# Optimization experiments

Measured on AMD Instinct MI355X. Metric: run time of the kernel, lower is better.

Reference implementation:

```python
import jax, jax.numpy as jnp
import numpy as np

STRIDES = (4.0, 8.0, 16.0, 32.0)
IMG = 1024.0


def setup_inputs() -> dict:
    key = jax.random.key(0)
    ks = jax.random.split(key, 10)
    N, P = 512, 128
    feat0 = jax.random.normal(ks[0], (2, 256, 256, 256), jnp.float32)
    feat1 = jax.random.normal(ks[1], (2, 256, 128, 128), jnp.float32)
    feat2 = jax.random.normal(ks[2], (2, 256, 64, 64), jnp.float32)
    feat3 = jax.random.normal(ks[3], (2, 256, 32, 32), jnp.float32)
    b = jax.random.randint(ks[4], (N,), 0, 2).astype(jnp.float32)
    x1 = jax.random.uniform(ks[5], (N,)) * 512.0
    y1 = jax.random.uniform(ks[6], (N,)) * 512.0
    w = 16.0 + jax.random.uniform(ks[7], (N,)) * 496.0
    h = 16.0 + jax.random.uniform(ks[8], (N,)) * 496.0
    rois = jnp.stack([b, x1, y1, x1 + w, y1 + h], axis=1)  # [N,5]
    points = jax.random.uniform(ks[9], (N, P, 2), jnp.float32)  # rel coords in [0,1]
    return {"feat0": feat0, "feat1": feat1, "feat2": feat2, "feat3": feat3,
            "rois": rois, "points": points}


def _sample_level(feat, coords, batch_idx, stride):
    # feat: [B,C,H,W]; coords: [N,P,2] absolute image (x,y); -> [N,C,P]
    B, C, H, W = feat.shape
    # grid_sample align_corners=False: pixel coord = img_coord/stride - 0.5
    px = coords[..., 0] / stride - 0.5
    py = coords[..., 1] / stride - 0.5
    x0 = jnp.floor(px)
    y0 = jnp.floor(py)
    wx = px - x0  # weight of x0+1
    wy = py - y0
    x0i = x0.astype(jnp.int32)
    y0i = y0.astype(jnp.int32)

    def gather(yi, xi):
        valid = (xi >= 0) & (xi < W) & (yi >= 0) & (yi < H)  # zeros padding
        xc = jnp.clip(xi, 0, W - 1)
        yc = jnp.clip(yi, 0, H - 1)
        v = feat[batch_idx[:, None], :, yc, xc]  # [N,P,C]
        return v * valid[..., None].astype(feat.dtype)

    v00 = gather(y0i, x0i)
    v01 = gather(y0i, x0i + 1)
    v10 = gather(y0i + 1, x0i)
    v11 = gather(y0i + 1, x0i + 1)
    wx = wx[..., None]
    wy = wy[..., None]
    out = (v00 * (1 - wx) * (1 - wy) + v01 * wx * (1 - wy)
           + v10 * (1 - wx) * wy + v11 * wx * wy)  # [N,P,C]
    return out.transpose(0, 2, 1)  # [N,C,P]


def reference(feat0, feat1, feat2, feat3, rois, points):
    batch_idx = rois[:, 0].astype(jnp.int32)  # [N]
    xy1 = rois[:, 1:3]  # [N,2]
    xy2 = rois[:, 3:5]
    # roi_point2img_coord: rel point -> absolute image coordinate
    coords = xy1[:, None, :] + points * (xy2 - xy1)[:, None, :]  # [N,P,2]
    feats = (feat0, feat1, feat2, feat3)
    per_level = [_sample_level(f, coords, batch_idx, s) for f, s in zip(feats, STRIDES)]
    return jnp.concatenate(per_level, axis=1)  # [N, sum(C)=1024, P]
```

## Files before the change

### kernel.cpp

```cpp
#include <hip/hip_runtime.h>
#include <hip/hip_bf16.h>

#define N_ROIS 512
#define P_PTS  128
#define C_CH   256
#define TILE_P 32
#define N_TILES (P_PTS / TILE_P)

#define L0_OFS 0
#define L1_OFS 33554432u
#define L2_OFS 41943040u
#define L3_OFS 44040192u
#define WS_ELEMS_NEEDED 44564480u

__device__ inline unsigned pack_bf16x2(float lo, float hi) {
    __hip_bfloat162 h = __float22bfloat162_rn(make_float2(lo, hi));
    unsigned r;
    __builtin_memcpy(&r, &h, 4);
    return r;
}
__device__ inline float bf16_lo(unsigned u) {
    return __uint_as_float(u << 16);
}
__device__ inline float bf16_hi(unsigned u) {
    return __uint_as_float(u & 0xffff0000u);
}

__global__ __launch_bounds__(256) void transpose_all_bf16(
    const float* __restrict__ f0, const float* __restrict__ f1,
    const float* __restrict__ f2, const float* __restrict__ f3,
    unsigned short* __restrict__ ws)
{
    const float* in; unsigned short* outp; int HW, pt;
    const int px = blockIdx.x;
    if (px < 32)        { in = f3; outp = ws + L3_OFS; HW = 1024;  pt = px; }
    else if (px < 160)  { in = f2; outp = ws + L2_OFS; HW = 4096;  pt = px - 32; }
    else if (px < 672)  { in = f1; outp = ws + L1_OFS; HW = 16384; pt = px - 160; }
    else                { in = f0; outp = ws + L0_OFS; HW = 65536; pt = px - 672; }

    __shared__ float tile[32][33];
    const int pix0 = pt * 32;
    const int c0   = blockIdx.y * 32;
    const int b    = blockIdx.z;
    in   += (size_t)b * C_CH * HW;
    outp += (size_t)b * C_CH * HW;
    const int tx = threadIdx.x;
    const int ty = threadIdx.y;

    #pragma unroll
    for (int i = 0; i < 32; i += 8)
        tile[ty + i][tx] = in[(size_t)(c0 + ty + i) * HW + pix0 + tx];
    __syncthreads();

    const int tid2 = ty * 32 + tx;
    const int wpix = tid2 >> 3;
    const int wq   = tid2 & 7;
    uint2 pk;
    pk.x = pack_bf16x2(tile[wq * 4 + 0][wpix], tile[wq * 4 + 1][wpix]);
    pk.y = pack_bf16x2(tile[wq * 4 + 2][wpix], tile[wq * 4 + 3][wpix]);
    *((uint2*)(outp + (size_t)(pix0 + wpix) * C_CH + c0 + wq * 4)) = pk;
}

__global__ __launch_bounds__(512, 6) void mpe_sample_v7(
    const unsigned short* __restrict__ fT,
    const float* __restrict__ rois, const float* __restrict__ points,
    float* __restrict__ out)
{
    const int n   = blockIdx.x & (N_ROIS - 1);
    const int lvl = 3 - (blockIdx.x >> 9);

    int H; float inv_stride; size_t lofs;
    if      (lvl == 0) { H = 256; inv_stride = 0.25f;    lofs = L0_OFS; }
    else if (lvl == 1) { H = 128; inv_stride = 0.125f;   lofs = L1_OFS; }
    else if (lvl == 2) { H = 64;  inv_stride = 0.0625f;  lofs = L2_OFS; }
    else               { H = 32;  inv_stride = 0.03125f; lofs = L3_OFS; }
    const int W  = H;
    const int HW = H * W;
    const unsigned short* feat = fT + lofs;

    __shared__ int4     s_off4[P_PTS];
    __shared__ float4   s_w4[P_PTS];
    __shared__ unsigned s_t2[TILE_P / 2][C_CH];

    const int tid = threadIdx.x;

    if (tid < P_PTS) {
        const int p = tid;
        const float bx = rois[n * 5 + 0];
        const float x1 = rois[n * 5 + 1];
        const float y1 = rois[n * 5 + 2];
        const float x2 = rois[n * 5 + 3];
        const float y2 = rois[n * 5 + 4];
        const float ptx = points[(n * P_PTS + p) * 2 + 0];
        const float pty = points[(n * P_PTS + p) * 2 + 1];

        const float cx = x1 + ptx * (x2 - x1);
        const float cy = y1 + pty * (y2 - y1);
        const float px = cx * inv_stride - 0.5f;
        const float py = cy * inv_stride - 0.5f;
        const float x0f = floorf(px);
        const float y0f = floorf(py);
        const float wx = px - x0f;
        const float wy = py - y0f;
        const int x0 = (int)x0f;
        const int y0 = (int)y0f;
        const int base = (int)bx * HW;

        int   o[4]; float w[4];
        #pragma unroll
        for (int k = 0; k < 4; ++k) {
            const int xi = x0 + (k & 1);
            const int yi = y0 + (k >> 1);
            const bool valid = (xi >= 0) & (xi < W) & (yi >= 0) & (yi < H);
            const int xc = min(max(xi, 0), W - 1);
            const int yc = min(max(yi, 0), H - 1);
            const float wk = ((k & 1) ? wx : 1.0f - wx) *
                             ((k >> 1) ? wy : 1.0f - wy);
            o[k] = base + yc * W + xc;
            w[k] = valid ? wk : 0.0f;
        }
        s_off4[p] = make_int4(o[0], o[1], o[2], o[3]);
        s_w4[p]   = make_float4(w[0], w[1], w[2], w[3]);
    }
    __syncthreads();

    const int wave = tid >> 6;
    const int lane = tid & 63;

    uint2 v[4][4];
    #pragma unroll
    for (int j = 0; j < 4; ++j) {
        const int4 o = s_off4[wave * 4 + j];
        v[j][0] = *((const uint2*)(feat + (size_t)o.x * C_CH) + lane);
        v[j][1] = *((const uint2*)(feat + (size_t)o.y * C_CH) + lane);
        v[j][2] = *((const uint2*)(feat + (size_t)o.z * C_CH) + lane);
        v[j][3] = *((const uint2*)(feat + (size_t)o.w * C_CH) + lane);
    }

    const int sc = tid >> 1;
    const int sh = tid & 1;
    float* const ob_base = out + ((size_t)n * 1024 + (size_t)lvl * 256 + sc) * P_PTS;

    for (int t = 0; t < N_TILES; ++t) {
        const int pbase = t * TILE_P + wave * 4;

        float a[4][4];
        #pragma unroll
        for (int j = 0; j < 4; ++j) {
            const float4 wj = s_w4[pbase + j];
            float ax = 0.f, ay = 0.f, az = 0.f, aw = 0.f;
            #pragma unroll
            for (int k = 0; k < 4; ++k) {
                const float wk = (k == 0) ? wj.x : (k == 1) ? wj.y : (k == 2) ? wj.z : wj.w;
                ax = fmaf(bf16_lo(v[j][k].x), wk, ax);
                ay = fmaf(bf16_hi(v[j][k].x), wk, ay);
                az = fmaf(bf16_lo(v[j][k].y), wk, az);
                aw = fmaf(bf16_hi(v[j][k].y), wk, aw);
            }
            a[j][0] = ax; a[j][1] = ay; a[j][2] = az; a[j][3] = aw;
        }
        #pragma unroll
        for (int m = 0; m < 2; ++m) {
            uint4 pk;
            pk.x = pack_bf16x2(a[2*m][0], a[2*m+1][0]);
            pk.y = pack_bf16x2(a[2*m][1], a[2*m+1][1]);
            pk.z = pack_bf16x2(a[2*m][2], a[2*m+1][2]);
            pk.w = pack_bf16x2(a[2*m][3], a[2*m+1][3]);
            *((uint4*)&s_t2[wave * 2 + m][lane * 4]) = pk;
        }

        if (t < N_TILES - 1) {
            const int pnext = pbase + TILE_P;
            #pragma unroll
            for (int j = 0; j < 4; ++j) {
                const int4 o = s_off4[pnext + j];
                v[j][0] = *((const uint2*)(feat + (size_t)o.x * C_CH) + lane);
                v[j][1] = *((const uint2*)(feat + (size_t)o.y * C_CH) + lane);
                v[j][2] = *((const uint2*)(feat + (size_t)o.z * C_CH) + lane);
                v[j][3] = *((const uint2*)(feat + (size_t)o.w * C_CH) + lane);
            }
        }

        asm volatile("s_waitcnt lgkmcnt(0)" ::: "memory");
        __builtin_amdgcn_s_barrier();
        __builtin_amdgcn_sched_barrier(0);

        float o16[16];
        #pragma unroll
        for (int q = 0; q < 8; ++q) {
            const unsigned u = s_t2[sh * 8 + q][sc];
            o16[2*q]   = bf16_lo(u);
            o16[2*q+1] = bf16_hi(u);
        }
        float* ob = ob_base + t * TILE_P + sh * 16;
        #pragma unroll
        for (int i4 = 0; i4 < 4; ++i4)
            *((float4*)(ob + i4 * 4)) =
                make_float4(o16[i4*4], o16[i4*4+1], o16[i4*4+2], o16[i4*4+3]);

        asm volatile("s_waitcnt lgkmcnt(0)" ::: "memory");
        __builtin_amdgcn_s_barrier();
        __builtin_amdgcn_sched_barrier(0);
    }
}

__global__ __launch_bounds__(256) void mpe_sample_nchw(
    const float* __restrict__ feat0, const float* __restrict__ feat1,
    const float* __restrict__ feat2, const float* __restrict__ feat3,
    const float* __restrict__ rois,  const float* __restrict__ points,
    float* __restrict__ out)
{
    const int blk = blockIdx.x;
    const int n   = blk >> 2;
    const int lvl = blk & 3;

    const float* feat;
    int H; float inv_stride;
    if      (lvl == 0) { feat = feat0; H = 256; inv_stride = 0.25f;    }
    else if (lvl == 1) { feat = feat1; H = 128; inv_stride = 0.125f;   }
    else if (lvl == 2) { feat = feat2; H = 64;  inv_stride = 0.0625f;  }
    else               { feat = feat3; H = 32;  inv_stride = 0.03125f; }
    const int W  = H;
    const int HW = H * W;

    __shared__ int   s_off[4][P_PTS];
    __shared__ float s_w[4][P_PTS];
    const int tid = threadIdx.x;

    if (tid < P_PTS) {
        const int p = tid;
        const float bx = rois[n * 5 + 0];
        const float x1 = rois[n * 5 + 1];
        const float y1 = rois[n * 5 + 2];
        const float x2 = rois[n * 5 + 3];
        const float y2 = rois[n * 5 + 4];
        const float ptx = points[(n * P_PTS + p) * 2 + 0];
        const float pty = points[(n * P_PTS + p) * 2 + 1];
        const float cx = x1 + ptx * (x2 - x1);
        const float cy = y1 + pty * (y2 - y1);
        const float px = cx * inv_stride - 0.5f;
        const float py = cy * inv_stride - 0.5f;
        const float x0f = floorf(px);
        const float y0f = floorf(py);
        const float wx = px - x0f;
        const float wy = py - y0f;
        const int x0 = (int)x0f;
        const int y0 = (int)y0f;
        const int base = (int)bx * C_CH * HW;
        #pragma unroll
        for (int k = 0; k < 4; ++k) {
            const int xi = x0 + (k & 1);
            const int yi = y0 + (k >> 1);
            const bool valid = (xi >= 0) & (xi < W) & (yi >= 0) & (yi < H);
            const int xc = min(max(xi, 0), W - 1);
            const int yc = min(max(yi, 0), H - 1);
            const float wk = ((k & 1) ? wx : 1.0f - wx) *
                             ((k >> 1) ? wy : 1.0f - wy);
            s_off[k][p] = base + yc * W + xc;
            s_w[k][p]   = valid ? wk : 0.0f;
        }
    }
    __syncthreads();

    const int p  = tid & (P_PTS - 1);
    const int c0 = tid >> 7;
    const int   off0 = s_off[0][p], off1 = s_off[1][p],
                off2 = s_off[2][p], off3 = s_off[3][p];
    const float w0 = s_w[0][p], w1 = s_w[1][p],
                w2 = s_w[2][p], w3 = s_w[3][p];
    const float* p0 = feat + off0 + c0 * HW;
    const float* p1 = feat + off1 + c0 * HW;
    const float* p2 = feat + off2 + c0 * HW;
    const float* p3 = feat + off3 + c0 * HW;
    float* po = out + ((size_t)n * 1024 + (size_t)lvl * 256 + c0) * P_PTS + p;
    const int step = 2 * HW;
    #pragma unroll 4
    for (int pass = 0; pass < C_CH / 2; ++pass) {
        *po = p0[0] * w0 + p1[0] * w1 + p2[0] * w2 + p3[0] * w3;
        p0 += step; p1 += step; p2 += step; p3 += step;
        po += 2 * P_PTS;
    }
}

extern "C" void kernel_launch(void* const* d_in, const int* in_sizes, int n_in,
                              void* d_out, int out_size, void* d_ws, size_t ws_size,
                              hipStream_t stream) {
    const float* feat0  = (const float*)d_in[0];
    const float* feat1  = (const float*)d_in[1];
    const float* feat2  = (const float*)d_in[2];
    const float* feat3  = (const float*)d_in[3];
    const float* rois   = (const float*)d_in[4];
    const float* points = (const float*)d_in[5];
    float* out = (float*)d_out;

    if (ws_size >= (size_t)WS_ELEMS_NEEDED * 2u) {
        unsigned short* fT = (unsigned short*)d_ws;
        transpose_all_bf16<<<dim3(2720, 8, 2), dim3(32, 8), 0, stream>>>(
            feat0, feat1, feat2, feat3, fT);
        mpe_sample_v7<<<dim3(N_ROIS * 4), dim3(512), 0, stream>>>(
            fT, rois, points, out);
    } else {
        mpe_sample_nchw<<<dim3(N_ROIS * 4), dim3(256), 0, stream>>>(
            feat0, feat1, feat2, feat3, rois, points, out);
    }
}
```

Before: 209.6 us.

## Fetch horizontally adjacent bilinear corners with one 16-byte load per row

Each sample point now issues two row loads instead of four corner loads. Every load reads the two adjacent pixels (x and x+1) of one row as a single 1KB contiguous span of channel-last bf16 data, 16 bytes per lane. The x-weights are folded to match a clamped base column, so edge cases stay correct. Each half-wave handles one pixel, and the two halves are combined with a cross-lane shuffle, which cuts the number of memory instructions and address computations. The cost is extra shuffle work and some remapped weight logic.

```diff
diff --git a/kernel.cpp b/kernel.cpp
--- a/kernel.cpp
+++ b/kernel.cpp
@@ -61,7 +61,7 @@
     *((uint2*)(outp + (size_t)(pix0 + wpix) * C_CH + c0 + wq * 4)) = pk;
 }
 
-__global__ __launch_bounds__(512, 6) void mpe_sample_v7(
+__global__ __launch_bounds__(512, 6) void mpe_sample_v8(
     const unsigned short* __restrict__ fT,
     const float* __restrict__ rois, const float* __restrict__ points,
     float* __restrict__ out)
@@ -78,7 +78,7 @@
     const int HW = H * W;
     const unsigned short* feat = fT + lofs;
 
-    __shared__ int4     s_off4[P_PTS];
+    __shared__ int2     s_off2[P_PTS];
     __shared__ float4   s_w4[P_PTS];
     __shared__ unsigned s_t2[TILE_P / 2][C_CH];
 
@@ -106,35 +106,38 @@
         const int y0 = (int)y0f;
         const int base = (int)bx * HW;
 
-        int   o[4]; float w[4];
-        #pragma unroll
-        for (int k = 0; k < 4; ++k) {
-            const int xi = x0 + (k & 1);
-            const int yi = y0 + (k >> 1);
-            const bool valid = (xi >= 0) & (xi < W) & (yi >= 0) & (yi < H);
-            const int xc = min(max(xi, 0), W - 1);
-            const int yc = min(max(yi, 0), H - 1);
-            const float wk = ((k & 1) ? wx : 1.0f - wx) *
-                             ((k >> 1) ? wy : 1.0f - wy);
-            o[k] = base + yc * W + xc;
-            w[k] = valid ? wk : 0.0f;
-        }
-        s_off4[p] = make_int4(o[0], o[1], o[2], o[3]);
-        s_w4[p]   = make_float4(w[0], w[1], w[2], w[3]);
+        const int xb = min(max(x0, 0), W - 2);
+        const bool xv0 = (x0 >= 0) & (x0 < W);
+        const bool xv1 = (x0 + 1 >= 0) & (x0 + 1 < W);
+        const int xc0 = min(max(x0, 0), W - 1);
+        const int xc1 = min(max(x0 + 1, 0), W - 1);
+        float xw0 = 0.f, xw1 = 0.f;
+        if (xv0) { if (xc0 == xb) xw0 += 1.0f - wx; else xw1 += 1.0f - wx; }
+        if (xv1) { if (xc1 == xb) xw0 += wx;        else xw1 += wx; }
+
+        const bool yv0 = (y0 >= 0) & (y0 < H);
+        const bool yv1 = (y0 + 1 >= 0) & (y0 + 1 < H);
+        const float yw0 = yv0 ? (1.0f - wy) : 0.0f;
+        const float yw1 = yv1 ? wy : 0.0f;
+        const int yc0 = min(max(y0, 0), H - 1);
+        const int yc1 = min(max(y0 + 1, 0), H - 1);
+
+        s_off2[p] = make_int2(base + yc0 * W + xb, base + yc1 * W + xb);
+        s_w4[p]   = make_float4(yw0 * xw0, yw0 * xw1, yw1 * xw0, yw1 * xw1);
     }
     __syncthreads();
 
     const int wave = tid >> 6;
     const int lane = tid & 63;
-
-    uint2 v[4][4];
+    const int h    = lane >> 5;
+    const int cl   = lane & 31;
+
+    uint4 v[4][2];
     #pragma unroll
     for (int j = 0; j < 4; ++j) {
-        const int4 o = s_off4[wave * 4 + j];
-        v[j][0] = *((const uint2*)(feat + (size_t)o.x * C_CH) + lane);
-        v[j][1] = *((const uint2*)(feat + (size_t)o.y * C_CH) + lane);
-        v[j][2] = *((const uint2*)(feat + (size_t)o.z * C_CH) + lane);
-        v[j][3] = *((const uint2*)(feat + (size_t)o.w * C_CH) + lane);
+        const int2 o = s_off2[wave * 4 + j];
+        v[j][0] = *((const uint4*)(feat + (size_t)o.x * C_CH) + lane);
+        v[j][1] = *((const uint4*)(feat + (size_t)o.y * C_CH) + lane);
     }
 
     const int sc = tid >> 1;
@@ -144,40 +147,47 @@
     for (int t = 0; t < N_TILES; ++t) {
         const int pbase = t * TILE_P + wave * 4;
 
-        float a[4][4];
+        float tt[4][8];
         #pragma unroll
         for (int j = 0; j < 4; ++j) {
             const float4 wj = s_w4[pbase + j];
-            float ax = 0.f, ay = 0.f, az = 0.f, aw = 0.f;
+            const float w0 = h ? wj.y : wj.x;
+            const float w1 = h ? wj.w : wj.z;
+            const uint4 a = v[j][0];
+            const uint4 b = v[j][1];
+            tt[j][0] = bf16_lo(a.x) * w0 + bf16_lo(b.x) * w1;
+            tt[j][1] = bf16_hi(a.x) * w0 + bf16_hi(b.x) * w1;
+            tt[j][2] = bf16_lo(a.y) * w0 + bf16_lo(b.y) * w1;
+            tt[j][3] = bf16_hi(a.y) * w0 + bf16_hi(b.y) * w1;
+            tt[j][4] = bf16_lo(a.z) * w0 + bf16_lo(b.z) * w1;
+            tt[j][5] = bf16_hi(a.z) * w0 + bf16_hi(b.z) * w1;
+            tt[j][6] = bf16_lo(a.w) * w0 + bf16_lo(b.w) * w1;
+            tt[j][7] = bf16_hi(a.w) * w0 + bf16_hi(b.w) * w1;
+        }
+        #pragma unroll
+        for (int j = 0; j < 4; ++j)
             #pragma unroll
-            for (int k = 0; k < 4; ++k) {
-                const float wk = (k == 0) ? wj.x : (k == 1) ? wj.y : (k == 2) ? wj.z : wj.w;
-                ax = fmaf(bf16_lo(v[j][k].x), wk, ax);
-                ay = fmaf(bf16_hi(v[j][k].x), wk, ay);
-                az = fmaf(bf16_lo(v[j][k].y), wk, az);
-                aw = fmaf(bf16_hi(v[j][k].y), wk, aw);
-            }
-            a[j][0] = ax; a[j][1] = ay; a[j][2] = az; a[j][3] = aw;
-        }
+            for (int c = 0; c < 8; ++c)
+                tt[j][c] += __shfl_xor(tt[j][c], 32);
+
         #pragma unroll
         for (int m = 0; m < 2; ++m) {
+            const int hb = h * 4;
             uint4 pk;
-            pk.x = pack_bf16x2(a[2*m][0], a[2*m+1][0]);
-            pk.y = pack_bf16x2(a[2*m][1], a[2*m+1][1]);
-            pk.z = pack_bf16x2(a[2*m][2], a[2*m+1][2]);
-            pk.w = pack_bf16x2(a[2*m][3], a[2*m+1][3]);
-            *((uint4*)&s_t2[wave * 2 + m][lane * 4]) = pk;
+            pk.x = pack_bf16x2(tt[2*m][hb+0], tt[2*m+1][hb+0]);
+            pk.y = pack_bf16x2(tt[2*m][hb+1], tt[2*m+1][hb+1]);
+            pk.z = pack_bf16x2(tt[2*m][hb+2], tt[2*m+1][hb+2]);
+            pk.w = pack_bf16x2(tt[2*m][hb+3], tt[2*m+1][hb+3]);
+            *((uint4*)&s_t2[wave * 2 + m][cl * 8 + hb]) = pk;
         }
 
         if (t < N_TILES - 1) {
             const int pnext = pbase + TILE_P;
             #pragma unroll
             for (int j = 0; j < 4; ++j) {
-                const int4 o = s_off4[pnext + j];
-                v[j][0] = *((const uint2*)(feat + (size_t)o.x * C_CH) + lane);
-                v[j][1] = *((const uint2*)(feat + (size_t)o.y * C_CH) + lane);
-                v[j][2] = *((const uint2*)(feat + (size_t)o.z * C_CH) + lane);
-                v[j][3] = *((const uint2*)(feat + (size_t)o.w * C_CH) + lane);
+                const int2 o = s_off2[pnext + j];
+                v[j][0] = *((const uint4*)(feat + (size_t)o.x * C_CH) + lane);
+                v[j][1] = *((const uint4*)(feat + (size_t)o.y * C_CH) + lane);
             }
         }
 
@@ -297,7 +307,7 @@
         unsigned short* fT = (unsigned short*)d_ws;
         transpose_all_bf16<<<dim3(2720, 8, 2), dim3(32, 8), 0, stream>>>(
             feat0, feat1, feat2, feat3, fT);
-        mpe_sample_v7<<<dim3(N_ROIS * 4), dim3(512), 0, stream>>>(
+        mpe_sample_v8<<<dim3(N_ROIS * 4), dim3(512), 0, stream>>>(
             fT, rois, points, out);
     } else {
         mpe_sample_nchw<<<dim3(N_ROIS * 4), dim3(256), 0, stream>>>(
```

Result: slower. 359.1 us (+71.3%).
